# Performance work log

Measured on AMD Instinct MI355X. Metric: run time of the kernel, lower is better.

Reference implementation:

```python
import jax, jax.numpy as jnp
import numpy as np

N_POL, N_TICK, N_COMM = 1000, 98000, 1000
N = N_POL + N_TICK + N_COMM
E = 1000000
EMB, HID, OUT, HEADS = 32, 64, 32, 4
EDGE_DIM = 5
N_STATES, N_SECTORS, N_INDUSTRIES = 50, 11, 74


def _p(k, shape, fan_in):
    return jax.random.normal(k, shape, jnp.float32) * (1.0 / np.sqrt(fan_in))


def setup_inputs():
    ks = jax.random.split(jax.random.key(0), 30)
    F1 = HID // HEADS
    d = {}
    d["edge_index"] = jax.random.randint(ks[0], (2, E), 0, N)
    d["edge_attr"] = jax.random.normal(ks[1], (E, EDGE_DIM), jnp.float32)
    d["pol_feat"] = jax.random.normal(ks[2], (N_POL, 7), jnp.float32)
    d["state_ids"] = jax.random.randint(ks[3], (N_POL,), 0, N_STATES)
    d["sector_ids"] = jax.random.randint(ks[4], (N_TICK,), 0, N_SECTORS)
    d["industry_ids"] = jax.random.randint(ks[5], (N_TICK,), 0, N_INDUSTRIES)
    d["comp_scalar"] = jax.random.normal(ks[6], (N_TICK, 1), jnp.float32)
    d["pol_W"] = _p(ks[7], (7, EMB), 7); d["pol_b"] = jnp.zeros((EMB,), jnp.float32)
    d["state_E"] = _p(ks[8], (N_STATES, EMB), 1)
    d["sector_E"] = _p(ks[9], (N_SECTORS, 8), 1)
    d["industry_E"] = _p(ks[10], (N_INDUSTRIES, 8), 1)
    d["comp_W"] = _p(ks[11], (17, EMB), 17); d["comp_b"] = jnp.zeros((EMB,), jnp.float32)
    d["comm_E"] = _p(ks[12], (N_COMM, EMB), 1)
    d["ln_g"] = jnp.ones((EMB,), jnp.float32); d["ln_b"] = jnp.zeros((EMB,), jnp.float32)
    d["c1_W"] = _p(ks[13], (EMB, HEADS * F1), EMB)
    d["c1_as"] = _p(ks[14], (HEADS, F1), F1); d["c1_ad"] = _p(ks[15], (HEADS, F1), F1)
    d["c1_eW"] = _p(ks[16], (EDGE_DIM, HEADS * F1), EDGE_DIM)
    d["c1_ae"] = _p(ks[17], (HEADS, F1), F1)
    d["c1_b"] = jnp.zeros((HID,), jnp.float32)
    d["c2_W"] = _p(ks[18], (HID, OUT), HID)
    d["c2_as"] = _p(ks[19], (1, OUT), OUT); d["c2_ad"] = _p(ks[20], (1, OUT), OUT)
    d["c2_eW"] = _p(ks[21], (EDGE_DIM, OUT), EDGE_DIM)
    d["c2_ae"] = _p(ks[22], (1, OUT), OUT)
    d["c2_b"] = jnp.zeros((OUT,), jnp.float32)
    return d


def _segment_softmax(logits, seg, num):
    # numerically stable per-destination softmax, per head (axis 0 is edges)
    m = jax.ops.segment_max(logits, seg, num_segments=num)
    ex = jnp.exp(logits - m[seg])
    s = jax.ops.segment_sum(ex, seg, num_segments=num)
    return ex / s[seg]


def _gat(x, src, dst, eattr, W, a_s, a_d, eW, a_e, b, heads, feat, concat):
    # PyG GATConv (eval mode): linear -> per-node alpha terms -> per-edge
    # leaky_relu -> destination softmax -> weighted scatter-sum.
    n = x.shape[0]
    h = (x @ W).reshape(n, heads, feat)                     # [N,H,F]
    a_src = jnp.sum(h * a_s, -1)                            # [N,H]
    a_dst = jnp.sum(h * a_d, -1)                            # [N,H]
    a_edge = jnp.sum((eattr @ eW).reshape(-1, heads, feat) * a_e, -1)  # [E,H]
    alpha = jax.nn.leaky_relu(a_src[src] + a_dst[dst] + a_edge, 0.2)
    alpha = _segment_softmax(alpha, dst, n)                 # [E,H]
    out = jax.ops.segment_sum(h[src] * alpha[..., None], dst, num_segments=n)
    out = out.reshape(n, heads * feat) if concat else out.mean(1)
    return out + b


def _forward(edge_index, edge_attr, pol_feat, state_ids, sector_ids, industry_ids,
             comp_scalar, pol_W, pol_b, state_E, sector_E, industry_E, comp_W,
             comp_b, comm_E, ln_g, ln_b, c1_W, c1_as, c1_ad, c1_eW, c1_ae, c1_b,
             c2_W, c2_as, c2_ad, c2_eW, c2_ae, c2_b):
    # node features
    pol = jax.nn.relu(pol_feat @ pol_W + pol_b) + state_E[state_ids]
    comp_in = jnp.concatenate([sector_E[sector_ids], industry_E[industry_ids], comp_scalar], 1)
    comp = jax.nn.relu(comp_in @ comp_W + comp_b)
    x = jnp.concatenate([pol, comp, comm_E], 0)             # [N,EMB]
    mu = jnp.mean(x, -1, keepdims=True)
    var = jnp.mean((x - mu) ** 2, -1, keepdims=True)
    x = (x - mu) / jnp.sqrt(var + 1e-5) * ln_g + ln_b
    # add self-loops with fill_value='mean' (per-dst mean of incoming edge_attr)
    src, dst = edge_index[0], edge_index[1]
    cnt = jax.ops.segment_sum(jnp.ones((E,), jnp.float32), dst, num_segments=N)
    loop_attr = jax.ops.segment_sum(edge_attr, dst, num_segments=N) / jnp.maximum(cnt, 1.0)[:, None]
    idx = jnp.arange(N)
    src2 = jnp.concatenate([src, idx]); dst2 = jnp.concatenate([dst, idx])
    ea2 = jnp.concatenate([edge_attr, loop_attr], 0)
    x = jax.nn.elu(_gat(x, src2, dst2, ea2, c1_W, c1_as, c1_ad, c1_eW, c1_ae, c1_b, HEADS, HID // HEADS, True))
    x = _gat(x, src2, dst2, ea2, c2_W, c2_as, c2_ad, c2_eW, c2_ae, c2_b, 1, OUT, False)
    return x


def reference(edge_index, edge_attr, pol_feat, state_ids, sector_ids, industry_ids,
              comp_scalar, pol_W, pol_b, state_E, sector_E, industry_E, comp_W,
              comp_b, comm_E, ln_g, ln_b, c1_W, c1_as, c1_ad, c1_eW, c1_ae, c1_b,
              c2_W, c2_as, c2_ad, c2_eW, c2_ae, c2_b):
    return _forward(edge_index, edge_attr, pol_feat, state_ids, sector_ids, industry_ids,
                    comp_scalar, pol_W, pol_b, state_E, sector_E, industry_E, comp_W,
                    comp_b, comm_E, ln_g, ln_b, c1_W, c1_as, c1_ad, c1_eW, c1_ae, c1_b,
                    c2_W, c2_as, c2_ad, c2_eW, c2_ae, c2_b)
```

## Files before the change

### kernel.cpp

```cpp
#include <hip/hip_runtime.h>
#include <math.h>

#define NPOL   1000
#define NTICK  98000
#define NCOMM  1000
#define NN     100000
#define NE     1000000
#define NE2    1100000
#define NPREBLK  3907
#define NFEATBLK 1563

__device__ __forceinline__ unsigned short f2bf(float v) {
    unsigned u = __float_as_uint(v);
    u += 0x7FFFu + ((u >> 16) & 1u);
    return (unsigned short)(u >> 16);
}
__device__ __forceinline__ float bf2f(unsigned short s) {
    return __uint_as_float(((unsigned)s) << 16);
}

__global__ void __launch_bounds__(256) k_pre(
    const int* __restrict__ ei, int* __restrict__ deg4, int* __restrict__ ord,
    const float* __restrict__ pol_feat, const int* __restrict__ state_ids,
    const int* __restrict__ sector_ids, const int* __restrict__ industry_ids,
    const float* __restrict__ comp_scalar,
    const float* __restrict__ pol_W, const float* __restrict__ pol_b,
    const float* __restrict__ state_E, const float* __restrict__ sector_E,
    const float* __restrict__ industry_E, const float* __restrict__ comp_W,
    const float* __restrict__ comp_b, const float* __restrict__ comm_E,
    const float* __restrict__ ln_g, const float* __restrict__ ln_b,
    const float* __restrict__ c1_W, const float* __restrict__ c1_as,
    const float* __restrict__ c1_ad,
    unsigned short* __restrict__ h1b, float* __restrict__ as1,
    float* __restrict__ ad1) {
    __shared__ float sW1[2048];
    __shared__ float sCompW[544];
    __shared__ float sPolW[224];
    __shared__ float sAs[64], sAd[64];
    __shared__ float sLg[32], sLb[32], sPb[32], sCb[32];
    int t = threadIdx.x;
    int e = blockIdx.x * 256 + t;
    int ret = 0, d = 0;
    bool hasEdge = (e < NE);
    if (hasEdge) {
        d = ei[NE + e];
        ret = atomicAdd(&deg4[(d << 2) | (e & 3)], 1);
    }
    if (blockIdx.x < NFEATBLK) {
        for (int i = t; i < 2048; i += 256) sW1[i] = c1_W[i];
        for (int i = t; i < 544; i += 256) sCompW[i] = comp_W[i];
        if (t < 224) sPolW[t] = pol_W[t];
        if (t < 64) { sAs[t] = c1_as[t]; sAd[t] = c1_ad[t]; }
        if (t < 32) { sLg[t] = ln_g[t]; sLb[t] = ln_b[t]; sPb[t] = pol_b[t]; sCb[t] = comp_b[t]; }
        __syncthreads();
        int tid = blockIdx.x * 256 + t;
        if (tid < 4 * NN) {
            int n = tid >> 2, q = tid & 3, jb = q * 8;
            float x[8];
            if (n < NPOL) {
                float f[7];
                #pragma unroll
                for (int i = 0; i < 7; ++i) f[i] = pol_feat[n * 7 + i];
                int sid = state_ids[n];
                #pragma unroll
                for (int jj = 0; jj < 8; ++jj) {
                    int j = jb + jj;
                    float v = sPb[j];
                    #pragma unroll
                    for (int i = 0; i < 7; ++i) v += f[i] * sPolW[i * 32 + j];
                    v = v > 0.f ? v : 0.f;
                    x[jj] = v + state_E[sid * 32 + j];
                }
            } else if (n < NPOL + NTICK) {
                int tt = n - NPOL;
                float f[17];
                int sec = sector_ids[tt], ind = industry_ids[tt];
                #pragma unroll
                for (int i = 0; i < 8; ++i) { f[i] = sector_E[sec * 8 + i]; f[8 + i] = industry_E[ind * 8 + i]; }
                f[16] = comp_scalar[tt];
                #pragma unroll
                for (int jj = 0; jj < 8; ++jj) {
                    int j = jb + jj;
                    float v = sCb[j];
                    #pragma unroll
                    for (int i = 0; i < 17; ++i) v += f[i] * sCompW[i * 32 + j];
                    x[jj] = v > 0.f ? v : 0.f;
                }
            } else {
                int c = n - (NPOL + NTICK);
                float4 a = *(const float4*)&comm_E[c * 32 + jb];
                float4 b = *(const float4*)&comm_E[c * 32 + jb + 4];
                x[0] = a.x; x[1] = a.y; x[2] = a.z; x[3] = a.w;
                x[4] = b.x; x[5] = b.y; x[6] = b.z; x[7] = b.w;
            }
            float s1 = 0.f;
            #pragma unroll
            for (int jj = 0; jj < 8; ++jj) s1 += x[jj];
            s1 += __shfl_xor(s1, 1); s1 += __shfl_xor(s1, 2);
            float mu = s1 * (1.f / 32.f);
            float s2 = 0.f;
            #pragma unroll
            for (int jj = 0; jj < 8; ++jj) { float dd = x[jj] - mu; s2 += dd * dd; }
            s2 += __shfl_xor(s2, 1); s2 += __shfl_xor(s2, 2);
            float inv = rsqrtf(s2 * (1.f / 32.f) + 1e-5f);
            #pragma unroll
            for (int jj = 0; jj < 8; ++jj) x[jj] = (x[jj] - mu) * inv * sLg[jb + jj] + sLb[jb + jj];
            float4 acc0 = {0,0,0,0}, acc1 = {0,0,0,0}, acc2 = {0,0,0,0}, acc3 = {0,0,0,0};
            int qb = (t & 63) & ~3;
            int jc = q * 16;
            #pragma unroll
            for (int p = 0; p < 4; ++p) {
                #pragma unroll
                for (int jj = 0; jj < 8; ++jj) {
                    float xs = __shfl(x[jj], qb + p, 64);
                    const float4* wr = (const float4*)&sW1[(p * 8 + jj) * 64 + jc];
                    float4 w0 = wr[0], w1 = wr[1], w2 = wr[2], w3 = wr[3];
                    acc0.x = fmaf(xs, w0.x, acc0.x); acc0.y = fmaf(xs, w0.y, acc0.y);
                    acc0.z = fmaf(xs, w0.z, acc0.z); acc0.w = fmaf(xs, w0.w, acc0.w);
                    acc1.x = fmaf(xs, w1.x, acc1.x); acc1.y = fmaf(xs, w1.y, acc1.y);
                    acc1.z = fmaf(xs, w1.z, acc1.z); acc1.w = fmaf(xs, w1.w, acc1.w);
                    acc2.x = fmaf(xs, w2.x, acc2.x); acc2.y = fmaf(xs, w2.y, acc2.y);
                    acc2.z = fmaf(xs, w2.z, acc2.z); acc2.w = fmaf(xs, w2.w, acc2.w);
                    acc3.x = fmaf(xs, w3.x, acc3.x); acc3.y = fmaf(xs, w3.y, acc3.y);
                    acc3.z = fmaf(xs, w3.z, acc3.z); acc3.w = fmaf(xs, w3.w, acc3.w);
                }
            }
            const float4* asv = (const float4*)sAs;
            const float4* adv = (const float4*)sAd;
            float4 a0 = asv[q * 4], a1 = asv[q * 4 + 1], a2 = asv[q * 4 + 2], a3 = asv[q * 4 + 3];
            float4 b0 = adv[q * 4], b1 = adv[q * 4 + 1], b2 = adv[q * 4 + 2], b3 = adv[q * 4 + 3];
            float av = acc0.x * a0.x + acc0.y * a0.y + acc0.z * a0.z + acc0.w * a0.w
                     + acc1.x * a1.x + acc1.y * a1.y + acc1.z * a1.z + acc1.w * a1.w
                     + acc2.x * a2.x + acc2.y * a2.y + acc2.z * a2.z + acc2.w * a2.w
                     + acc3.x * a3.x + acc3.y * a3.y + acc3.z * a3.z + acc3.w * a3.w;
            float dv = acc0.x * b0.x + acc0.y * b0.y + acc0.z * b0.z + acc0.w * b0.w
                     + acc1.x * b1.x + acc1.y * b1.y + acc1.z * b1.z + acc1.w * b1.w
                     + acc2.x * b2.x + acc2.y * b2.y + acc2.z * b2.z + acc2.w * b2.w
                     + acc3.x * b3.x + acc3.y * b3.y + acc3.z * b3.z + acc3.w * b3.w;
            as1[tid] = av;
            ad1[tid] = dv;
            uint4 w1o, w2o;
            w1o.x = (unsigned)f2bf(acc0.x) | ((unsigned)f2bf(acc0.y) << 16);
            w1o.y = (unsigned)f2bf(acc0.z) | ((unsigned)f2bf(acc0.w) << 16);
            w1o.z = (unsigned)f2bf(acc1.x) | ((unsigned)f2bf(acc1.y) << 16);
            w1o.w = (unsigned)f2bf(acc1.z) | ((unsigned)f2bf(acc1.w) << 16);
            w2o.x = (unsigned)f2bf(acc2.x) | ((unsigned)f2bf(acc2.y) << 16);
            w2o.y = (unsigned)f2bf(acc2.z) | ((unsigned)f2bf(acc2.w) << 16);
            w2o.z = (unsigned)f2bf(acc3.x) | ((unsigned)f2bf(acc3.y) << 16);
            w2o.w = (unsigned)f2bf(acc3.z) | ((unsigned)f2bf(acc3.w) << 16);
            unsigned short* hp = h1b + (unsigned)n * 64u + (unsigned)jc;
            *(uint4*)hp = w1o;
            *(uint4*)(hp + 8) = w2o;
        }
    }
    if (hasEdge) ord[e] = ret;
}

__global__ void k_scan1(const int4* __restrict__ deg4, int* __restrict__ degS,
                        int* __restrict__ row_start, int* __restrict__ bsum) {
    __shared__ int tmp[1024];
    int i = blockIdx.x * 1024 + threadIdx.x;
    int s = 0;
    if (i < NN) {
        int4 d4 = deg4[i];
        s = d4.x + d4.y + d4.z + d4.w;
        degS[i] = s;
    }
    int v = (i < NN) ? s + 1 : 0;
    tmp[threadIdx.x] = v;
    __syncthreads();
    for (int off = 1; off < 1024; off <<= 1) {
        int u = (threadIdx.x >= off) ? tmp[threadIdx.x - off] : 0;
        __syncthreads();
        tmp[threadIdx.x] += u;
        __syncthreads();
    }
    if (i < NN) row_start[i] = tmp[threadIdx.x] - v;
    if (threadIdx.x == 1023) bsum[blockIdx.x] = tmp[1023];
}
__global__ void k_scan2(int* __restrict__ bsum, int nb) {
    __shared__ int tmp[128];
    int t = threadIdx.x;
    int v = (t < nb) ? bsum[t] : 0;
    tmp[t] = v;
    __syncthreads();
    for (int off = 1; off < 128; off <<= 1) {
        int u = (t >= off) ? tmp[t - off] : 0;
        __syncthreads();
        tmp[t] += u;
        __syncthreads();
    }
    if (t < nb) bsum[t] = tmp[t] - v;
}
__global__ void k_scan3(int* __restrict__ row_start, const int* __restrict__ bsum,
                        const int4* __restrict__ deg4, int4* __restrict__ row4) {
    int i = blockIdx.x * blockDim.x + threadIdx.x;
    if (i >= NN) return;
    int rs = row_start[i] + bsum[i >> 10];
    row_start[i] = rs;
    int4 d4 = deg4[i];
    int r0 = rs + 1;
    row4[i] = make_int4(r0, r0 + d4.x, r0 + d4.x + d4.y, r0 + d4.x + d4.y + d4.z);
}

__global__ void __launch_bounds__(256) k_fill(
    const int* __restrict__ ei, const float* __restrict__ edge_attr,
    const int* __restrict__ row4, const int* __restrict__ ord,
    const float* __restrict__ c1_eW, const float* __restrict__ c1_ae,
    const float* __restrict__ c2_eW, const float* __restrict__ c2_ae,
    float4* __restrict__ rec) {
    __shared__ float we1s[20];
    __shared__ float we2s[5];
    int t = threadIdx.x;
    if (t < 20) {
        int d = t >> 2, h = t & 3;
        float s = 0.f;
        for (int f = 0; f < 16; ++f) s += c1_eW[d * 64 + h * 16 + f] * c1_ae[h * 16 + f];
        we1s[t] = s;
    } else if (t >= 32 && t < 37) {
        int d = t - 32;
        float s = 0.f;
        for (int f = 0; f < 32; ++f) s += c2_eW[d * 32 + f] * c2_ae[f];
        we2s[d] = s;
    }
    __syncthreads();
    int e = blockIdx.x * 256 + t;
    if (e >= NE) return;
    int s = ei[e], d = ei[NE + e];
    int pos = row4[(d << 2) | (e & 3)] + ord[e];
    float a[5];
    #pragma unroll
    for (int k = 0; k < 5; ++k) a[k] = edge_attr[e * 5 + k];
    float e0 = 0.f, e1 = 0.f, e2 = 0.f, e3 = 0.f, e4 = 0.f;
    #pragma unroll
    for (int k = 0; k < 5; ++k) {
        e0 += a[k] * we1s[k * 4 + 0];
        e1 += a[k] * we1s[k * 4 + 1];
        e2 += a[k] * we1s[k * 4 + 2];
        e3 += a[k] * we1s[k * 4 + 3];
        e4 += a[k] * we2s[k];
    }
    unsigned u01 = (unsigned)f2bf(e0) | ((unsigned)f2bf(e1) << 16);
    unsigned u23 = (unsigned)f2bf(e2) | ((unsigned)f2bf(e3) << 16);
    rec[pos] = make_float4(__int_as_float(s), __uint_as_float(u01),
                           __uint_as_float(u23), e4);
}

__global__ void __launch_bounds__(256) k_agg1(
    const int* __restrict__ row_start, const int* __restrict__ degS,
    float4* __restrict__ rec,
    const float* __restrict__ as1, const float* __restrict__ ad1,
    const unsigned short* __restrict__ h1b, const float* __restrict__ c1_b,
    unsigned short* __restrict__ x1b) {
    __shared__ float pT[4][2][32][4];
    __shared__ int   srcT[4][2][32];
    int wid = threadIdx.x >> 6;
    int lane = threadIdx.x & 63;
    int half = lane >> 5;
    int j = lane & 31;
    int h = j >> 3;
    int n = blockIdx.x * 8 + wid * 2 + half;
    int base = row_start[n];
    int dg   = degS[n];
    const float4* as1v4 = (const float4*)as1;
    const float4* ad1v4 = (const float4*)ad1;
    float4 adv = ad1v4[n];
    float4 asv = as1v4[n];
    unsigned uself = *(const unsigned*)(h1b + (unsigned)n * 64u + 2u * (unsigned)j);

    float ssum = 0.f, acc0 = 0.f, acc1 = 0.f;
    float aes0 = 0.f, aes1 = 0.f, aes2 = 0.f, aes3 = 0.f, ae2sum = 0.f;

    for (int i0 = 0; i0 < dg; i0 += 32) {
        int clen = dg - i0; if (clen > 32) clen = 32;
        int idx = i0 + j;
        if (idx < dg) {
            float4 r = rec[base + 1 + idx];
            int s = __float_as_int(r.x);
            unsigned u01 = __float_as_uint(r.y), u23 = __float_as_uint(r.z);
            float ae0  = bf2f((unsigned short)u01);
            float ae1v = bf2f((unsigned short)(u01 >> 16));
            float ae2v = bf2f((unsigned short)u23);
            float ae3v = bf2f((unsigned short)(u23 >> 16));
            float4 av = as1v4[s];
            float l0 = av.x + adv.x + ae0;  l0 = l0 > 0.f ? l0 : 0.2f * l0;
            float l1 = av.y + adv.y + ae1v; l1 = l1 > 0.f ? l1 : 0.2f * l1;
            float l2 = av.z + adv.z + ae2v; l2 = l2 > 0.f ? l2 : 0.2f * l2;
            float l3 = av.w + adv.w + ae3v; l3 = l3 > 0.f ? l3 : 0.2f * l3;
            float4 q = make_float4(__expf(l0), __expf(l1), __expf(l2), __expf(l3));
            *(float4*)&pT[wid][half][j][0] = q;
            srcT[wid][half][j] = s;
            aes0 += ae0; aes1 += ae1v; aes2 += ae2v; aes3 += ae3v;
            ae2sum += r.w;
        }
        int i = 0;
        for (; i + 4 <= clen; i += 4) {
            int s0 = srcT[wid][half][i],     s1 = srcT[wid][half][i + 1];
            int s2 = srcT[wid][half][i + 2], s3 = srcT[wid][half][i + 3];
            float q0 = pT[wid][half][i][h],     q1 = pT[wid][half][i + 1][h];
            float q2 = pT[wid][half][i + 2][h], q3 = pT[wid][half][i + 3][h];
            unsigned g0 = *(const unsigned*)(h1b + (unsigned)s0 * 64u + 2u * (unsigned)j);
            unsigned g1 = *(const unsigned*)(h1b + (unsigned)s1 * 64u + 2u * (unsigned)j);
            unsigned g2 = *(const unsigned*)(h1b + (unsigned)s2 * 64u + 2u * (unsigned)j);
            unsigned g3 = *(const unsigned*)(h1b + (unsigned)s3 * 64u + 2u * (unsigned)j);
            ssum += (q0 + q1) + (q2 + q3);
            acc0 = fmaf(q0, bf2f((unsigned short)g0),
                   fmaf(q1, bf2f((unsigned short)g1),
                   fmaf(q2, bf2f((unsigned short)g2),
                   fmaf(q3, bf2f((unsigned short)g3), acc0))));
            acc1 = fmaf(q0, bf2f((unsigned short)(g0 >> 16)),
                   fmaf(q1, bf2f((unsigned short)(g1 >> 16)),
                   fmaf(q2, bf2f((unsigned short)(g2 >> 16)),
                   fmaf(q3, bf2f((unsigned short)(g3 >> 16)), acc1))));
        }
        for (; i < clen; ++i) {
            int s0 = srcT[wid][half][i];
            float q0 = pT[wid][half][i][h];
            unsigned g0 = *(const unsigned*)(h1b + (unsigned)s0 * 64u + 2u * (unsigned)j);
            ssum += q0;
            acc0 = fmaf(q0, bf2f((unsigned short)g0), acc0);
            acc1 = fmaf(q0, bf2f((unsigned short)(g0 >> 16)), acc1);
        }
    }
    #pragma unroll
    for (int m = 1; m < 32; m <<= 1) {
        aes0 += __shfl_xor(aes0, m);
        aes1 += __shfl_xor(aes1, m);
        aes2 += __shfl_xor(aes2, m);
        aes3 += __shfl_xor(aes3, m);
        ae2sum += __shfl_xor(ae2sum, m);
    }
    float invd = 1.f / fmaxf((float)dg, 1.f);
    float aesh = (h == 0) ? aes0 : (h == 1) ? aes1 : (h == 2) ? aes2 : aes3;
    float adh  = (h == 0) ? adv.x : (h == 1) ? adv.y : (h == 2) ? adv.z : adv.w;
    float ash  = (h == 0) ? asv.x : (h == 1) ? asv.y : (h == 2) ? asv.z : asv.w;
    float ls = ash + adh + aesh * invd;
    ls = ls > 0.f ? ls : 0.2f * ls;
    float ps = __expf(ls);
    ssum += ps;
    acc0 = fmaf(ps, bf2f((unsigned short)uself), acc0);
    acc1 = fmaf(ps, bf2f((unsigned short)(uself >> 16)), acc1);
    if (j == 0) {
        rec[base] = make_float4(__int_as_float(n), 0.f, 0.f, ae2sum * invd);
    }
    float inv_s = 1.f / ssum;
    float x0 = acc0 * inv_s + c1_b[2 * j];
    float x1 = acc1 * inv_s + c1_b[2 * j + 1];
    x0 = (x0 > 0.f) ? x0 : (__expf(x0) - 1.f);
    x1 = (x1 > 0.f) ? x1 : (__expf(x1) - 1.f);
    unsigned w = (unsigned)f2bf(x0) | ((unsigned)f2bf(x1) << 16);
    *(unsigned*)(x1b + (unsigned)n * 64u + 2u * (unsigned)j) = w;
}

__global__ void __launch_bounds__(256) k_mid(
    const unsigned short* __restrict__ x1b, const float* __restrict__ c2_W,
    const float* __restrict__ c2_as, const float* __restrict__ c2_ad,
    unsigned short* __restrict__ h2b, float* __restrict__ as2,
    float* __restrict__ ad2) {
    int wave = (blockIdx.x * 256 + threadIdx.x) >> 6;
    int lane = threadIdx.x & 63;
    int half = lane >> 5, j = lane & 31;
    int n = wave * 2 + half;
    unsigned u = *(const unsigned*)(x1b + (unsigned)n * 64u + j * 2u);
    float acc = 0.f;
    #pragma unroll
    for (int t = 0; t < 32; ++t) {
        unsigned xu = (unsigned)__shfl((int)u, half * 32 + t, 64);
        float x0 = bf2f((unsigned short)xu);
        float x1 = bf2f((unsigned short)(xu >> 16));
        acc = fmaf(x0, c2_W[(2 * t) * 32 + j], acc);
        acc = fmaf(x1, c2_W[(2 * t + 1) * 32 + j], acc);
    }
    float a = acc * c2_as[j], b = acc * c2_ad[j];
    #pragma unroll
    for (int m = 16; m > 0; m >>= 1) {
        a += __shfl_xor(a, m, 64);
        b += __shfl_xor(b, m, 64);
    }
    if (j == 0) { as2[n] = a; ad2[n] = b; }
    h2b[(unsigned)n * 32u + j] = f2bf(acc);
}

__global__ void __launch_bounds__(256) k_agg2(
    const int* __restrict__ row_start, const int* __restrict__ degS,
    const float4* __restrict__ rec, const float* __restrict__ as2,
    const float* __restrict__ ad2, const unsigned short* __restrict__ h2b,
    const float* __restrict__ c2_b, float* __restrict__ out) {
    __shared__ float2 spT[8][32];
    int t = threadIdx.x;
    int half = t >> 5;
    int l32 = t & 31;
    int n = blockIdx.x * 8 + half;
    int base = row_start[n];
    int len = degS[n] + 1;
    float ad2n = ad2[n];
    float ssum = 0.f, acc = 0.f;
    for (int i0 = 0; i0 < len; i0 += 32) {
        int clen = len - i0; if (clen > 32) clen = 32;
        int idx = i0 + l32;
        float p = 0.f; int s = 0;
        if (idx < len) {
            float4 r = rec[base + idx];
            s = __float_as_int(r.x);
            float l = as2[s] + ad2n + r.w;
            l = l > 0.f ? l : 0.2f * l;
            p = __expf(l);
        }
        ssum += p;
        spT[half][l32] = make_float2(__int_as_float(s), p);
        int i = 0;
        for (; i + 4 <= clen; i += 4) {
            float2 e0 = spT[half][i],     e1 = spT[half][i + 1];
            float2 e2 = spT[half][i + 2], e3 = spT[half][i + 3];
            int s0 = __float_as_int(e0.x), s1 = __float_as_int(e1.x);
            int s2 = __float_as_int(e2.x), s3 = __float_as_int(e3.x);
            float g0 = bf2f(h2b[(unsigned)s0 * 32u + l32]);
            float g1 = bf2f(h2b[(unsigned)s1 * 32u + l32]);
            float g2 = bf2f(h2b[(unsigned)s2 * 32u + l32]);
            float g3 = bf2f(h2b[(unsigned)s3 * 32u + l32]);
            acc = fmaf(e0.y, g0, fmaf(e1.y, g1, fmaf(e2.y, g2, fmaf(e3.y, g3, acc))));
        }
        for (; i < clen; ++i) {
            float2 e0 = spT[half][i];
            int s0 = __float_as_int(e0.x);
            acc = fmaf(e0.y, bf2f(h2b[(unsigned)s0 * 32u + l32]), acc);
        }
    }
    #pragma unroll
    for (int m = 1; m < 32; m <<= 1) ssum += __shfl_xor(ssum, m, 32);
    out[(size_t)n * 32 + l32] = acc / ssum + c2_b[l32];
}

extern "C" void kernel_launch(void* const* d_in, const int* in_sizes, int n_in,
                              void* d_out, int out_size, void* d_ws, size_t ws_size,
                              hipStream_t stream) {
    const int*   edge_index  = (const int*)  d_in[0];
    const float* edge_attr   = (const float*)d_in[1];
    const float* pol_feat    = (const float*)d_in[2];
    const int*   state_ids   = (const int*)  d_in[3];
    const int*   sector_ids  = (const int*)  d_in[4];
    const int*   industry_ids= (const int*)  d_in[5];
    const float* comp_scalar = (const float*)d_in[6];
    const float* pol_W   = (const float*)d_in[7];
    const float* pol_b   = (const float*)d_in[8];
    const float* state_E = (const float*)d_in[9];
    const float* sector_E= (const float*)d_in[10];
    const float* industry_E=(const float*)d_in[11];
    const float* comp_W  = (const float*)d_in[12];
    const float* comp_b  = (const float*)d_in[13];
    const float* comm_E  = (const float*)d_in[14];
    const float* ln_g    = (const float*)d_in[15];
    const float* ln_b    = (const float*)d_in[16];
    const float* c1_W    = (const float*)d_in[17];
    const float* c1_as   = (const float*)d_in[18];
    const float* c1_ad   = (const float*)d_in[19];
    const float* c1_eW   = (const float*)d_in[20];
    const float* c1_ae   = (const float*)d_in[21];
    const float* c1_b    = (const float*)d_in[22];
    const float* c2_W    = (const float*)d_in[23];
    const float* c2_as   = (const float*)d_in[24];
    const float* c2_ad   = (const float*)d_in[25];
    const float* c2_eW   = (const float*)d_in[26];
    const float* c2_ae   = (const float*)d_in[27];
    const float* c2_b    = (const float*)d_in[28];
    float* out = (float*)d_out;

    char* ws = (char*)d_ws;
    size_t off = 0;
    auto alloc = [&](size_t bytes) { void* p = ws + off; off += (bytes + 255) & ~(size_t)255; return p; };
    int*   deg4      = (int*)  alloc((size_t)NN * 16);
    int*   ord       = (int*)  alloc((size_t)NE * 4);
    int*   row_start = (int*)  alloc(NN * 4);
    int*   degS      = (int*)  alloc(NN * 4);
    int*   row4      = (int*)  alloc((size_t)NN * 16);
    int*   bsum      = (int*)  alloc(128 * 4);
    float4* rec      = (float4*)alloc((size_t)NE2 * 16);
    unsigned short* h1b = (unsigned short*)alloc((size_t)NN * 64 * 2);
    float* as1       = (float*)alloc((size_t)NN * 4 * 4);
    float* ad1       = (float*)alloc((size_t)NN * 4 * 4);
    unsigned short* x1b = (unsigned short*)alloc((size_t)NN * 64 * 2);
    unsigned short* h2b = (unsigned short*)alloc((size_t)NN * 32 * 2);
    float* as2       = (float*)alloc(NN * 4);
    float* ad2       = (float*)alloc(NN * 4);
    (void)ws_size; (void)in_sizes; (void)n_in; (void)out_size;

    hipMemsetAsync(deg4, 0, (size_t)NN * 16, stream);

    k_pre<<<NPREBLK, 256, 0, stream>>>(
        edge_index, deg4, ord,
        pol_feat, state_ids, sector_ids, industry_ids, comp_scalar,
        pol_W, pol_b, state_E, sector_E, industry_E, comp_W, comp_b, comm_E,
        ln_g, ln_b, c1_W, c1_as, c1_ad, h1b, as1, ad1);
    int nblk = (NN + 1023) / 1024;
    k_scan1<<<nblk, 1024, 0, stream>>>((const int4*)deg4, degS, row_start, bsum);
    k_scan2<<<1, 128, 0, stream>>>(bsum, nblk);
    k_scan3<<<(NN + 255) / 256, 256, 0, stream>>>(row_start, bsum, (const int4*)deg4, (int4*)row4);
    k_fill<<<(NE + 255) / 256, 256, 0, stream>>>(
        edge_index, edge_attr, row4, ord, c1_eW, c1_ae, c2_eW, c2_ae, rec);
    k_agg1<<<NN / 8, 256, 0, stream>>>(
        row_start, degS, rec, as1, ad1, h1b, c1_b, x1b);
    k_mid<<<(NN / 2) / 4, 256, 0, stream>>>(
        x1b, c2_W, c2_as, c2_ad, h2b, as2, ad2);
    k_agg2<<<NN / 8, 256, 0, stream>>>(
        row_start, degS, rec, as2, ad2, h2b, c2_b, out);
}
```

Before: 187.3 us.

## Use single degree counter per node and process three edges per thread in k_pre

Replaces the 4-way split degree counters (deg4/row4) with a single per-node degree array, removing the degS and row4 buffers and simplifying the scan and fill kernels. k_pre is shrunk to the feature-block count, with each thread handling three edges' atomic degree increments, issued after the shared weight load so the loads overlap. This cuts memory traffic for the counter arrays and removes the blocks that only did atomics, but puts four times as many atomics on each counter, which may add contention on high-degree nodes.

```diff
diff --git a/kernel.cpp b/kernel.cpp
--- a/kernel.cpp
+++ b/kernel.cpp
@@ -7,8 +7,8 @@
 #define NN     100000
 #define NE     1000000
 #define NE2    1100000
-#define NPREBLK  3907
-#define NFEATBLK 1563
+#define NPREBLK  1563
+#define PRET     400128
 
 __device__ __forceinline__ unsigned short f2bf(float v) {
     unsigned u = __float_as_uint(v);
@@ -20,7 +20,7 @@
 }
 
 __global__ void __launch_bounds__(256) k_pre(
-    const int* __restrict__ ei, int* __restrict__ deg4, int* __restrict__ ord,
+    const int* __restrict__ ei, int* __restrict__ deg, int* __restrict__ ord,
     const float* __restrict__ pol_feat, const int* __restrict__ state_ids,
     const int* __restrict__ sector_ids, const int* __restrict__ industry_ids,
     const float* __restrict__ comp_scalar,
@@ -39,134 +39,129 @@
     __shared__ float sAs[64], sAd[64];
     __shared__ float sLg[32], sLb[32], sPb[32], sCb[32];
     int t = threadIdx.x;
-    int e = blockIdx.x * 256 + t;
-    int ret = 0, d = 0;
-    bool hasEdge = (e < NE);
-    if (hasEdge) {
-        d = ei[NE + e];
-        ret = atomicAdd(&deg4[(d << 2) | (e & 3)], 1);
-    }
-    if (blockIdx.x < NFEATBLK) {
-        for (int i = t; i < 2048; i += 256) sW1[i] = c1_W[i];
-        for (int i = t; i < 544; i += 256) sCompW[i] = comp_W[i];
-        if (t < 224) sPolW[t] = pol_W[t];
-        if (t < 64) { sAs[t] = c1_as[t]; sAd[t] = c1_ad[t]; }
-        if (t < 32) { sLg[t] = ln_g[t]; sLb[t] = ln_b[t]; sPb[t] = pol_b[t]; sCb[t] = comp_b[t]; }
-        __syncthreads();
-        int tid = blockIdx.x * 256 + t;
-        if (tid < 4 * NN) {
-            int n = tid >> 2, q = tid & 3, jb = q * 8;
-            float x[8];
-            if (n < NPOL) {
-                float f[7];
+    int tid = blockIdx.x * 256 + t;
+    int e0 = tid, e1 = tid + PRET, e2 = tid + 2 * PRET;
+    bool b1 = e1 < NE, b2 = e2 < NE;
+    int d0 = ei[NE + e0];
+    int d1 = b1 ? ei[NE + e1] : 0;
+    int d2 = b2 ? ei[NE + e2] : 0;
+    for (int i = t; i < 2048; i += 256) sW1[i] = c1_W[i];
+    for (int i = t; i < 544; i += 256) sCompW[i] = comp_W[i];
+    if (t < 224) sPolW[t] = pol_W[t];
+    if (t < 64) { sAs[t] = c1_as[t]; sAd[t] = c1_ad[t]; }
+    if (t < 32) { sLg[t] = ln_g[t]; sLb[t] = ln_b[t]; sPb[t] = pol_b[t]; sCb[t] = comp_b[t]; }
+    __syncthreads();
+    int r0 = atomicAdd(&deg[d0], 1);
+    int r1 = b1 ? atomicAdd(&deg[d1], 1) : 0;
+    int r2 = b2 ? atomicAdd(&deg[d2], 1) : 0;
+    if (tid < 4 * NN) {
+        int n = tid >> 2, q = tid & 3, jb = q * 8;
+        float x[8];
+        if (n < NPOL) {
+            float f[7];
+            #pragma unroll
+            for (int i = 0; i < 7; ++i) f[i] = pol_feat[n * 7 + i];
+            int sid = state_ids[n];
+            #pragma unroll
+            for (int jj = 0; jj < 8; ++jj) {
+                int j = jb + jj;
+                float v = sPb[j];
                 #pragma unroll
-                for (int i = 0; i < 7; ++i) f[i] = pol_feat[n * 7 + i];
-                int sid = state_ids[n];
+                for (int i = 0; i < 7; ++i) v += f[i] * sPolW[i * 32 + j];
+                v = v > 0.f ? v : 0.f;
+                x[jj] = v + state_E[sid * 32 + j];
+            }
+        } else if (n < NPOL + NTICK) {
+            int tt = n - NPOL;
+            float f[17];
+            int sec = sector_ids[tt], ind = industry_ids[tt];
+            #pragma unroll
+            for (int i = 0; i < 8; ++i) { f[i] = sector_E[sec * 8 + i]; f[8 + i] = industry_E[ind * 8 + i]; }
+            f[16] = comp_scalar[tt];
+            #pragma unroll
+            for (int jj = 0; jj < 8; ++jj) {
+                int j = jb + jj;
+                float v = sCb[j];
                 #pragma unroll
-                for (int jj = 0; jj < 8; ++jj) {
-                    int j = jb + jj;
-                    float v = sPb[j];
-                    #pragma unroll
-                    for (int i = 0; i < 7; ++i) v += f[i] * sPolW[i * 32 + j];
-                    v = v > 0.f ? v : 0.f;
-                    x[jj] = v + state_E[sid * 32 + j];
-                }
-            } else if (n < NPOL + NTICK) {
-                int tt = n - NPOL;
-                float f[17];
-                int sec = sector_ids[tt], ind = industry_ids[tt];
-                #pragma unroll
-                for (int i = 0; i < 8; ++i) { f[i] = sector_E[sec * 8 + i]; f[8 + i] = industry_E[ind * 8 + i]; }
-                f[16] = comp_scalar[tt];
-                #pragma unroll
-                for (int jj = 0; jj < 8; ++jj) {
-                    int j = jb + jj;
-                    float v = sCb[j];
-                    #pragma unroll
-                    for (int i = 0; i < 17; ++i) v += f[i] * sCompW[i * 32 + j];
-                    x[jj] = v > 0.f ? v : 0.f;
-                }
-            } else {
-                int c = n - (NPOL + NTICK);
-                float4 a = *(const float4*)&comm_E[c * 32 + jb];
-                float4 b = *(const float4*)&comm_E[c * 32 + jb + 4];
-                x[0] = a.x; x[1] = a.y; x[2] = a.z; x[3] = a.w;
-                x[4] = b.x; x[5] = b.y; x[6] = b.z; x[7] = b.w;
+                for (int i = 0; i < 17; ++i) v += f[i] * sCompW[i * 32 + j];
+                x[jj] = v > 0.f ? v : 0.f;
             }
-            float s1 = 0.f;
+        } else {
+            int c = n - (NPOL + NTICK);
+            float4 a = *(const float4*)&comm_E[c * 32 + jb];
+            float4 b = *(const float4*)&comm_E[c * 32 + jb + 4];
+            x[0] = a.x; x[1] = a.y; x[2] = a.z; x[3] = a.w;
+            x[4] = b.x; x[5] = b.y; x[6] = b.z; x[7] = b.w;
+        }
+        float s1 = 0.f;
+        #pragma unroll
+        for (int jj = 0; jj < 8; ++jj) s1 += x[jj];
+        s1 += __shfl_xor(s1, 1); s1 += __shfl_xor(s1, 2);
+        float mu = s1 * (1.f / 32.f);
+        float s2 = 0.f;
+        #pragma unroll
+        for (int jj = 0; jj < 8; ++jj) { float dd = x[jj] - mu; s2 += dd * dd; }
+        s2 += __shfl_xor(s2, 1); s2 += __shfl_xor(s2, 2);
+        float inv = rsqrtf(s2 * (1.f / 32.f) + 1e-5f);
+        #pragma unroll
+        for (int jj = 0; jj < 8; ++jj) x[jj] = (x[jj] - mu) * inv * sLg[jb + jj] + sLb[jb + jj];
+        float4 acc0 = {0,0,0,0}, acc1 = {0,0,0,0}, acc2 = {0,0,0,0}, acc3 = {0,0,0,0};
+        int qb = (t & 63) & ~3;
+        int jc = q * 16;
+        #pragma unroll
+        for (int p = 0; p < 4; ++p) {
             #pragma unroll
-            for (int jj = 0; jj < 8; ++jj) s1 += x[jj];
-            s1 += __shfl_xor(s1, 1); s1 += __shfl_xor(s1, 2);
-            float mu = s1 * (1.f / 32.f);
-            float s2 = 0.f;
-            #pragma unroll
-            for (int jj = 0; jj < 8; ++jj) { float dd = x[jj] - mu; s2 += dd * dd; }
-            s2 += __shfl_xor(s2, 1); s2 += __shfl_xor(s2, 2);
-            float inv = rsqrtf(s2 * (1.f / 32.f) + 1e-5f);
-            #pragma unroll
-            for (int jj = 0; jj < 8; ++jj) x[jj] = (x[jj] - mu) * inv * sLg[jb + jj] + sLb[jb + jj];
-            float4 acc0 = {0,0,0,0}, acc1 = {0,0,0,0}, acc2 = {0,0,0,0}, acc3 = {0,0,0,0};
-            int qb = (t & 63) & ~3;
-            int jc = q * 16;
-            #pragma unroll
-            for (int p = 0; p < 4; ++p) {
-                #pragma unroll
-                for (int jj = 0; jj < 8; ++jj) {
-                    float xs = __shfl(x[jj], qb + p, 64);
-                    const float4* wr = (const float4*)&sW1[(p * 8 + jj) * 64 + jc];
-                    float4 w0 = wr[0], w1 = wr[1], w2 = wr[2], w3 = wr[3];
-                    acc0.x = fmaf(xs, w0.x, acc0.x); acc0.y = fmaf(xs, w0.y, acc0.y);
-                    acc0.z = fmaf(xs, w0.z, acc0.z); acc0.w = fmaf(xs, w0.w, acc0.w);
-                    acc1.x = fmaf(xs, w1.x, acc1.x); acc1.y = fmaf(xs, w1.y, acc1.y);
-                    acc1.z = fmaf(xs, w1.z, acc1.z); acc1.w = fmaf(xs, w1.w, acc1.w);
-                    acc2.x = fmaf(xs, w2.x, acc2.x); acc2.y = fmaf(xs, w2.y, acc2.y);
-                    acc2.z = fmaf(xs, w2.z, acc2.z); acc2.w = fmaf(xs, w2.w, acc2.w);
-                    acc3.x = fmaf(xs, w3.x, acc3.x); acc3.y = fmaf(xs, w3.y, acc3.y);
-                    acc3.z = fmaf(xs, w3.z, acc3.z); acc3.w = fmaf(xs, w3.w, acc3.w);
-                }
+            for (int jj = 0; jj < 8; ++jj) {
+                float xs = __shfl(x[jj], qb + p, 64);
+                const float4* wr = (const float4*)&sW1[(p * 8 + jj) * 64 + jc];
+                float4 w0 = wr[0], w1 = wr[1], w2 = wr[2], w3 = wr[3];
+                acc0.x = fmaf(xs, w0.x, acc0.x); acc0.y = fmaf(xs, w0.y, acc0.y);
+                acc0.z = fmaf(xs, w0.z, acc0.z); acc0.w = fmaf(xs, w0.w, acc0.w);
+                acc1.x = fmaf(xs, w1.x, acc1.x); acc1.y = fmaf(xs, w1.y, acc1.y);
+                acc1.z = fmaf(xs, w1.z, acc1.z); acc1.w = fmaf(xs, w1.w, acc1.w);
+                acc2.x = fmaf(xs, w2.x, acc2.x); acc2.y = fmaf(xs, w2.y, acc2.y);
+                acc2.z = fmaf(xs, w2.z, acc2.z); acc2.w = fmaf(xs, w2.w, acc2.w);
+                acc3.x = fmaf(xs, w3.x, acc3.x); acc3.y = fmaf(xs, w3.y, acc3.y);
+                acc3.z = fmaf(xs, w3.z, acc3.z); acc3.w = fmaf(xs, w3.w, acc3.w);
             }
-            const float4* asv = (const float4*)sAs;
-            const float4* adv = (const float4*)sAd;
-            float4 a0 = asv[q * 4], a1 = asv[q * 4 + 1], a2 = asv[q * 4 + 2], a3 = asv[q * 4 + 3];
-            float4 b0 = adv[q * 4], b1 = adv[q * 4 + 1], b2 = adv[q * 4 + 2], b3 = adv[q * 4 + 3];
-            float av = acc0.x * a0.x + acc0.y * a0.y + acc0.z * a0.z + acc0.w * a0.w
-                     + acc1.x * a1.x + acc1.y * a1.y + acc1.z * a1.z + acc1.w * a1.w
-                     + acc2.x * a2.x + acc2.y * a2.y + acc2.z * a2.z + acc2.w * a2.w
-                     + acc3.x * a3.x + acc3.y * a3.y + acc3.z * a3.z + acc3.w * a3.w;
-            float dv = acc0.x * b0.x + acc0.y * b0.y + acc0.z * b0.z + acc0.w * b0.w
-                     + acc1.x * b1.x + acc1.y * b1.y + acc1.z * b1.z + acc1.w * b1.w
-                     + acc2.x * b2.x + acc2.y * b2.y + acc2.z * b2.z + acc2.w * b2.w
-                     + acc3.x * b3.x + acc3.y * b3.y + acc3.z * b3.z + acc3.w * b3.w;
-            as1[tid] = av;
-            ad1[tid] = dv;
-            uint4 w1o, w2o;
-            w1o.x = (unsigned)f2bf(acc0.x) | ((unsigned)f2bf(acc0.y) << 16);
-            w1o.y = (unsigned)f2bf(acc0.z) | ((unsigned)f2bf(acc0.w) << 16);
-            w1o.z = (unsigned)f2bf(acc1.x) | ((unsigned)f2bf(acc1.y) << 16);
-            w1o.w = (unsigned)f2bf(acc1.z) | ((unsigned)f2bf(acc1.w) << 16);
-            w2o.x = (unsigned)f2bf(acc2.x) | ((unsigned)f2bf(acc2.y) << 16);
-            w2o.y = (unsigned)f2bf(acc2.z) | ((unsigned)f2bf(acc2.w) << 16);
-            w2o.z = (unsigned)f2bf(acc3.x) | ((unsigned)f2bf(acc3.y) << 16);
-            w2o.w = (unsigned)f2bf(acc3.z) | ((unsigned)f2bf(acc3.w) << 16);
-            unsigned short* hp = h1b + (unsigned)n * 64u + (unsigned)jc;
-            *(uint4*)hp = w1o;
-            *(uint4*)(hp + 8) = w2o;
-        }
-    }
-    if (hasEdge) ord[e] = ret;
-}
-
-__global__ void k_scan1(const int4* __restrict__ deg4, int* __restrict__ degS,
-                        int* __restrict__ row_start, int* __restrict__ bsum) {
+        }
+        const float4* asv = (const float4*)sAs;
+        const float4* adv = (const float4*)sAd;
+        float4 a0 = asv[q * 4], a1 = asv[q * 4 + 1], a2 = asv[q * 4 + 2], a3 = asv[q * 4 + 3];
+        float4 b0 = adv[q * 4], b1v = adv[q * 4 + 1], b2v = adv[q * 4 + 2], b3 = adv[q * 4 + 3];
+        float av = acc0.x * a0.x + acc0.y * a0.y + acc0.z * a0.z + acc0.w * a0.w
+                 + acc1.x * a1.x + acc1.y * a1.y + acc1.z * a1.z + acc1.w * a1.w
+                 + acc2.x * a2.x + acc2.y * a2.y + acc2.z * a2.z + acc2.w * a2.w
+                 + acc3.x * a3.x + acc3.y * a3.y + acc3.z * a3.z + acc3.w * a3.w;
+        float dv = acc0.x * b0.x + acc0.y * b0.y + acc0.z * b0.z + acc0.w * b0.w
+                 + acc1.x * b1v.x + acc1.y * b1v.y + acc1.z * b1v.z + acc1.w * b1v.w
+                 + acc2.x * b2v.x + acc2.y * b2v.y + acc2.z * b2v.z + acc2.w * b2v.w
+                 + acc3.x * b3.x + acc3.y * b3.y + acc3.z * b3.z + acc3.w * b3.w;
+        as1[tid] = av;
+        ad1[tid] = dv;
+        uint4 w1o, w2o;
+        w1o.x = (unsigned)f2bf(acc0.x) | ((unsigned)f2bf(acc0.y) << 16);
+        w1o.y = (unsigned)f2bf(acc0.z) | ((unsigned)f2bf(acc0.w) << 16);
+        w1o.z = (unsigned)f2bf(acc1.x) | ((unsigned)f2bf(acc1.y) << 16);
+        w1o.w = (unsigned)f2bf(acc1.z) | ((unsigned)f2bf(acc1.w) << 16);
+        w2o.x = (unsigned)f2bf(acc2.x) | ((unsigned)f2bf(acc2.y) << 16);
+        w2o.y = (unsigned)f2bf(acc2.z) | ((unsigned)f2bf(acc2.w) << 16);
+        w2o.z = (unsigned)f2bf(acc3.x) | ((unsigned)f2bf(acc3.y) << 16);
+        w2o.w = (unsigned)f2bf(acc3.z) | ((unsigned)f2bf(acc3.w) << 16);
+        unsigned short* hp = h1b + (unsigned)n * 64u + (unsigned)jc;
+        *(uint4*)hp = w1o;
+        *(uint4*)(hp + 8) = w2o;
+    }
+    ord[e0] = r0;
+    if (b1) ord[e1] = r1;
+    if (b2) ord[e2] = r2;
+}
+
+__global__ void k_scan1(const int* __restrict__ deg, int* __restrict__ row_start,
+                        int* __restrict__ bsum) {
     __shared__ int tmp[1024];
     int i = blockIdx.x * 1024 + threadIdx.x;
-    int s = 0;
-    if (i < NN) {
-        int4 d4 = deg4[i];
-        s = d4.x + d4.y + d4.z + d4.w;
-        degS[i] = s;
-    }
-    int v = (i < NN) ? s + 1 : 0;
+    int v = (i < NN) ? deg[i] + 1 : 0;
     tmp[threadIdx.x] = v;
     __syncthreads();
     for (int off = 1; off < 1024; off <<= 1) {
@@ -192,20 +187,14 @@
     }
     if (t < nb) bsum[t] = tmp[t] - v;
 }
-__global__ void k_scan3(int* __restrict__ row_start, const int* __restrict__ bsum,
-                        const int4* __restrict__ deg4, int4* __restrict__ row4) {
+__global__ void k_scan3(int* __restrict__ row_start, const int* __restrict__ bsum) {
     int i = blockIdx.x * blockDim.x + threadIdx.x;
-    if (i >= NN) return;
-    int rs = row_start[i] + bsum[i >> 10];
-    row_start[i] = rs;
-    int4 d4 = deg4[i];
-    int r0 = rs + 1;
-    row4[i] = make_int4(r0, r0 + d4.x, r0 + d4.x + d4.y, r0 + d4.x + d4.y + d4.z);
+    if (i < NN) row_start[i] += bsum[i >> 10];
 }
 
 __global__ void __launch_bounds__(256) k_fill(
     const int* __restrict__ ei, const float* __restrict__ edge_attr,
-    const int* __restrict__ row4, const int* __restrict__ ord,
+    const int* __restrict__ row_start, const int* __restrict__ ord,
     const float* __restrict__ c1_eW, const float* __restrict__ c1_ae,
     const float* __restrict__ c2_eW, const float* __restrict__ c2_ae,
     float4* __restrict__ rec) {
@@ -227,7 +216,7 @@
     int e = blockIdx.x * 256 + t;
     if (e >= NE) return;
     int s = ei[e], d = ei[NE + e];
-    int pos = row4[(d << 2) | (e & 3)] + ord[e];
+    int pos = row_start[d] + 1 + ord[e];
     float a[5];
     #pragma unroll
     for (int k = 0; k < 5; ++k) a[k] = edge_attr[e * 5 + k];
@@ -247,7 +236,7 @@
 }
 
 __global__ void __launch_bounds__(256) k_agg1(
-    const int* __restrict__ row_start, const int* __restrict__ degS,
+    const int* __restrict__ row_start, const int* __restrict__ deg,
     float4* __restrict__ rec,
     const float* __restrict__ as1, const float* __restrict__ ad1,
     const unsigned short* __restrict__ h1b, const float* __restrict__ c1_b,
@@ -261,7 +250,7 @@
     int h = j >> 3;
     int n = blockIdx.x * 8 + wid * 2 + half;
     int base = row_start[n];
-    int dg   = degS[n];
+    int dg   = deg[n];
     const float4* as1v4 = (const float4*)as1;
     const float4* ad1v4 = (const float4*)ad1;
     float4 adv = ad1v4[n];
@@ -382,7 +371,7 @@
 }
 
 __global__ void __launch_bounds__(256) k_agg2(
-    const int* __restrict__ row_start, const int* __restrict__ degS,
+    const int* __restrict__ row_start, const int* __restrict__ deg,
     const float4* __restrict__ rec, const float* __restrict__ as2,
     const float* __restrict__ ad2, const unsigned short* __restrict__ h2b,
     const float* __restrict__ c2_b, float* __restrict__ out) {
@@ -392,7 +381,7 @@
     int l32 = t & 31;
     int n = blockIdx.x * 8 + half;
     int base = row_start[n];
-    int len = degS[n] + 1;
+    int len = deg[n] + 1;
     float ad2n = ad2[n];
     float ssum = 0.f, acc = 0.f;
     for (int i0 = 0; i0 < len; i0 += 32) {
@@ -468,11 +457,9 @@
     char* ws = (char*)d_ws;
     size_t off = 0;
     auto alloc = [&](size_t bytes) { void* p = ws + off; off += (bytes + 255) & ~(size_t)255; return p; };
-    int*   deg4      = (int*)  alloc((size_t)NN * 16);
+    int*   deg       = (int*)  alloc(NN * 4);
     int*   ord       = (int*)  alloc((size_t)NE * 4);
     int*   row_start = (int*)  alloc(NN * 4);
-    int*   degS      = (int*)  alloc(NN * 4);
-    int*   row4      = (int*)  alloc((size_t)NN * 16);
     int*   bsum      = (int*)  alloc(128 * 4);
     float4* rec      = (float4*)alloc((size_t)NE2 * 16);
     unsigned short* h1b = (unsigned short*)alloc((size_t)NN * 64 * 2);
@@ -484,23 +471,23 @@
     float* ad2       = (float*)alloc(NN * 4);
     (void)ws_size; (void)in_sizes; (void)n_in; (void)out_size;
 
-    hipMemsetAsync(deg4, 0, (size_t)NN * 16, stream);
+    hipMemsetAsync(deg, 0, NN * 4, stream);
 
     k_pre<<<NPREBLK, 256, 0, stream>>>(
-        edge_index, deg4, ord,
+        edge_index, deg, ord,
         pol_feat, state_ids, sector_ids, industry_ids, comp_scalar,
         pol_W, pol_b, state_E, sector_E, industry_E, comp_W, comp_b, comm_E,
         ln_g, ln_b, c1_W, c1_as, c1_ad, h1b, as1, ad1);
     int nblk = (NN + 1023) / 1024;
-    k_scan1<<<nblk, 1024, 0, stream>>>((const int4*)deg4, degS, row_start, bsum);
+    k_scan1<<<nblk, 1024, 0, stream>>>(deg, row_start, bsum);
     k_scan2<<<1, 128, 0, stream>>>(bsum, nblk);
-    k_scan3<<<(NN + 255) / 256, 256, 0, stream>>>(row_start, bsum, (const int4*)deg4, (int4*)row4);
+    k_scan3<<<(NN + 255) / 256, 256, 0, stream>>>(row_start, bsum);
     k_fill<<<(NE + 255) / 256, 256, 0, stream>>>(
-        edge_index, edge_attr, row4, ord, c1_eW, c1_ae, c2_eW, c2_ae, rec);
+        edge_index, edge_attr, row_start, ord, c1_eW, c1_ae, c2_eW, c2_ae, rec);
     k_agg1<<<NN / 8, 256, 0, stream>>>(
-        row_start, degS, rec, as1, ad1, h1b, c1_b, x1b);
+        row_start, deg, rec, as1, ad1, h1b, c1_b, x1b);
     k_mid<<<(NN / 2) / 4, 256, 0, stream>>>(
         x1b, c2_W, c2_as, c2_ad, h2b, as2, ad2);
     k_agg2<<<NN / 8, 256, 0, stream>>>(
-        row_start, degS, rec, as2, ad2, h2b, c2_b, out);
-}
+        row_start, deg, rec, as2, ad2, h2b, c2_b, out);
+}
```

Result: faster. 182.6 us (-2.5%).
